# Optimization experiments

Hardware: AMD Instinct MI355X
Metric: run time of the kernel (lower is better)

Reference implementation:

```python
import jax, jax.numpy as jnp
import numpy as np

P = 32    # cardinality (number of parallel paths)
C = 256   # block input/output channels
D = 4     # bottleneck width per path
EPS = 1e-3  # Keras BatchNormalization default epsilon


def setup_inputs() -> dict:
    key = jax.random.key(0)
    ks = jax.random.split(key, 24)
    def nrm(k, shape, s=0.05):
        return jax.random.normal(k, shape, dtype=jnp.float32) * s
    inp = {}
    inp["x"] = jax.random.normal(ks[0], (8, 56, 56, C), dtype=jnp.float32)
    # conv weights/biases, stacked over the path axis P
    inp["W1"] = nrm(ks[1], (P, C, D))          # 1x1 conv C->4
    inp["B1"] = nrm(ks[2], (P, D))
    inp["W2"] = nrm(ks[3], (P, 3, 3, D, D))    # 3x3 conv 4->4 (HWIO)
    inp["B2"] = nrm(ks[4], (P, D))
    inp["W3"] = nrm(ks[5], (P, D, C))          # 1x1 conv 4->256
    inp["B3"] = nrm(ks[6], (P, C))
    # BatchNorm (inference): gamma, beta, moving mean, moving var per stage
    inp["G1"]  = 1.0 + nrm(ks[7], (P, D));  inp["Be1"] = nrm(ks[8], (P, D))
    inp["M1"]  = nrm(ks[9], (P, D));        inp["V1"]  = 1.0 + 0.1 * jax.random.uniform(ks[10], (P, D), dtype=jnp.float32)
    inp["G2"]  = 1.0 + nrm(ks[11], (P, D)); inp["Be2"] = nrm(ks[12], (P, D))
    inp["M2"]  = nrm(ks[13], (P, D));       inp["V2"]  = 1.0 + 0.1 * jax.random.uniform(ks[14], (P, D), dtype=jnp.float32)
    inp["G3"]  = 1.0 + nrm(ks[15], (P, C)); inp["Be3"] = nrm(ks[16], (P, C))
    inp["M3"]  = nrm(ks[17], (P, C));       inp["V3"]  = 1.0 + 0.1 * jax.random.uniform(ks[18], (P, C), dtype=jnp.float32)
    return inp


def _bn(x, g, b, m, v):
    # inference batch-norm: affine over channel axis
    return g * (x - m) * jax.lax.rsqrt(v + EPS) + b


def _path(x, w1, b1, g1, be1, m1, v1, w2, b2, g2, be2, m2, v2, w3, b3, g3, be3, m3, v3):
    h = jnp.einsum('nhwc,cd->nhwd', x, w1) + b1            # 1x1 conv C->D
    h = jax.nn.relu(_bn(h, g1, be1, m1, v1))
    h = jax.lax.conv_general_dilated(
        h, w2, window_strides=(1, 1), padding='SAME',
        dimension_numbers=('NHWC', 'HWIO', 'NHWC')) + b2   # 3x3 conv D->D
    h = jax.nn.relu(_bn(h, g2, be2, m2, v2))
    h = jnp.einsum('nhwd,dc->nhwc', h, w3) + b3            # 1x1 conv D->C
    h = jax.nn.relu(_bn(h, g3, be3, m3, v3))
    return h  # Dropout(0.2) is identity at inference


def reference(x, W1, B1, G1, Be1, M1, V1, W2, B2, G2, Be2, M2, V2, W3, B3, G3, Be3, M3, V3):
    # vmap over the 32 cardinality paths; x is shared (in_axes=None)
    paths = jax.vmap(_path, in_axes=(None,) + (0,) * 18)(
        x, W1, B1, G1, Be1, M1, V1, W2, B2, G2, Be2, M2, V2, W3, B3, G3, Be3, M3, V3)
    return jax.nn.relu(paths.sum(axis=0) + x)
```

## Files before the change

### kernel.cpp

```cpp
#include <hip/hip_runtime.h>

#define BATCH 8
#define HH 56
#define WW 56
#define NPOS (BATCH*HH*WW)
#define C 256
#define P 32
#define D 4
#define J 128
#define EPS 1e-3f
#define H2S 136

typedef __attribute__((ext_vector_type(8))) short bf16x8_t;
typedef __attribute__((ext_vector_type(4))) float f32x4_t;

__device__ __forceinline__ unsigned short f2bf(float f) {
    union { float f; unsigned int i; } v; v.f = f;
    unsigned int r = v.i + 0x7fffu + ((v.i >> 16) & 1u);
    return (unsigned short)(r >> 16);
}
__device__ __forceinline__ uint2 pack4_trunc(float4 v) {
    uint2 r;
    r.x = __builtin_amdgcn_perm(__float_as_uint(v.y), __float_as_uint(v.x), 0x07060302u);
    r.y = __builtin_amdgcn_perm(__float_as_uint(v.w), __float_as_uint(v.z), 0x07060302u);
    return r;
}

__global__ __launch_bounds__(256) void fold_params(
    const float* __restrict__ W1, const float* __restrict__ B1,
    const float* __restrict__ W2, const float* __restrict__ B2,
    const float* __restrict__ W3, const float* __restrict__ B3,
    const float* __restrict__ G1, const float* __restrict__ Be1,
    const float* __restrict__ M1, const float* __restrict__ V1,
    const float* __restrict__ G2, const float* __restrict__ Be2,
    const float* __restrict__ M2, const float* __restrict__ V2,
    const float* __restrict__ G3, const float* __restrict__ Be3,
    const float* __restrict__ M3, const float* __restrict__ V3,
    unsigned short* __restrict__ W1bf, float* __restrict__ b1f,
    float* __restrict__ w2q, float* __restrict__ b2t,
    unsigned short* __restrict__ WB, unsigned short* __restrict__ zb)
{
    int idx = blockIdx.x * 256 + threadIdx.x;

    if (idx < C*J) {
        int j = idx >> 8, c = idx & 255;
        int p = j >> 2, d = j & 3;
        float s = G1[j] * rsqrtf(V1[j] + EPS);
        W1bf[idx] = f2bf(W1[(p*C + c)*D + d] * s);
        return;
    }
    idx -= C*J;
    if (idx < J) {
        float s = G1[idx] * rsqrtf(V1[idx] + EPS);
        b1f[idx] = B1[idx] * s + Be1[idx] - M1[idx] * s;
        return;
    }
    idx -= J;
    if (idx < 9*D*D*P) {
        int do_ = idx & 3, p = (idx >> 2) & 31;
        int r2 = idx >> 7, di = r2 & 3, k9 = r2 >> 2;
        int j = p*4 + do_;
        float s = G2[j] * rsqrtf(V2[j] + EPS);
        w2q[idx] = W2[((p*9 + k9)*4 + di)*4 + do_] * s;
        return;
    }
    idx -= 9*D*D*P;
    if (idx < J) {
        int do_ = idx >> 5, p = idx & 31;
        int j = p*4 + do_;
        float s = G2[j] * rsqrtf(V2[j] + EPS);
        b2t[idx] = B2[j] * s + Be2[j] - M2[j] * s;
        return;
    }
    idx -= J;
    if (idx < P*C*8) {
        int s8 = idx & 7;
        int c = (idx >> 3) & 255;
        int p = idx >> 11;
        float sc = G3[p*C + c] * rsqrtf(V3[p*C + c] + EPS);
        float v = 0.f;
        if (s8 < 4)       v = W3[(p*D + s8)*C + c] * sc;
        else if (s8 == 4) v = B3[p*C + c] * sc + Be3[p*C + c] - M3[p*C + c] * sc;
        WB[idx] = f2bf(v);
        return;
    }
    idx -= P*C*8;
    if (idx < 8) { zb[idx] = 0; return; }
}

__global__ __launch_bounds__(256) void fused_all(
    const float* __restrict__ x, const unsigned short* __restrict__ W1bf,
    const float* __restrict__ b1f, const float* __restrict__ w2q,
    const float* __restrict__ b2t, const unsigned short* __restrict__ WB,
    const unsigned short* __restrict__ zb, float* __restrict__ out)
{
    __shared__ unsigned short xs[64*256];
    __shared__ unsigned short h1L[64*132];
    __shared__ float w2s[4608];
    __shared__ float bs[128];
    __shared__ float b1s[128];
    __shared__ unsigned short h2s[32*H2S];

    const int tid = threadIdx.x;
    int bxx = blockIdx.x;
    const int xb = bxx % 7;  bxx /= 7;
    const int yb = bxx % 14; const int b = bxx / 14;
    const int wid = tid >> 6, l = tid & 63, l15 = l & 15, quad = l >> 4;
    const int j0w = wid * 32;

    union bu { uint4 u; bf16x8_t v; };
    bu aw[2][8];
#pragma unroll
    for (int jf = 0; jf < 2; ++jf) {
        int row = j0w + jf*16 + l15;
#pragma unroll
        for (int kc = 0; kc < 8; ++kc)
            aw[jf][kc].u = *(const uint4*)&W1bf[row*C + kc*32 + quad*8];
    }

    for (int i = tid; i < 4608; i += 256) w2s[i] = w2q[i];
    if (tid < 128) { bs[tid] = b2t[tid]; b1s[tid] = b1f[tid]; }

#pragma unroll
    for (int it = 0; it < 8; ++it) {
        int idx = it*256 + tid;
        int pos = idx >> 5, g = idx & 31;
        uint4 st; st.x = 0u; st.y = 0u; st.z = 0u; st.w = 0u;
        if (pos < 60) {
            int hy = pos / 10, hx = pos - hy*10;
            int gy = yb*4 + hy - 1, gx = xb*8 + hx - 1;
            if (gy >= 0 && gy < HH && gx >= 0 && gx < WW) {
                const float* xp = &x[(size_t)((b*HH + gy)*WW + gx) * C + g*8];
                float4 v0 = *(const float4*)xp;
                float4 v1 = *(const float4*)(xp + 4);
                uint2 p0 = pack4_trunc(v0), p1 = pack4_trunc(v1);
                st.x = p0.x; st.y = p0.y; st.z = p1.x; st.w = p1.y;
            }
        }
        *(uint4*)&xs[pos*256 + ((g ^ (pos & 7)) * 8)] = st;
    }
    __syncthreads();

#pragma unroll
    for (int mt = 0; mt < 4; ++mt) {
        const int row = mt*16 + l15;
        int hy = (row * 205) >> 11;
        int hx = row - hy*10;
        int gy = yb*4 + hy - 1, gx = xb*8 + hx - 1;
        unsigned mask = (row < 60 && gy >= 0 && gy < HH && gx >= 0 && gx < WW)
                        ? 0xFFFFFFFFu : 0u;
        f32x4_t acc0 = (f32x4_t){0.f,0.f,0.f,0.f};
        f32x4_t acc1 = (f32x4_t){0.f,0.f,0.f,0.f};
#pragma unroll
        for (int kc = 0; kc < 8; ++kc) {
            int g = (kc*4 + quad) ^ (row & 7);
            bf16x8_t bb = *(const bf16x8_t*)&xs[row*256 + g*8];
            acc0 = __builtin_amdgcn_mfma_f32_16x16x32_bf16(aw[0][kc].v, bb, acc0, 0, 0, 0);
            acc1 = __builtin_amdgcn_mfma_f32_16x16x32_bf16(aw[1][kc].v, bb, acc1, 0, 0, 0);
        }
#pragma unroll
        for (int jf = 0; jf < 2; ++jf) {
            const f32x4_t a = jf ? acc1 : acc0;
            int jb = j0w + jf*16 + quad*4;
            float4 bias = *(const float4*)&b1s[jb];
            float v0 = fmaxf(a[0] + bias.x, 0.f);
            float v1 = fmaxf(a[1] + bias.y, 0.f);
            float v2 = fmaxf(a[2] + bias.z, 0.f);
            float v3 = fmaxf(a[3] + bias.w, 0.f);
            uint2 o;
            o.x = ((unsigned int)f2bf(v0) | ((unsigned int)f2bf(v1) << 16)) & mask;
            o.y = ((unsigned int)f2bf(v2) | ((unsigned int)f2bf(v3) << 16)) & mask;
            *(uint2*)&h1L[row*132 + jb] = o;
        }
    }
    __syncthreads();

    const int p = tid & 31;
    const int slot = tid >> 5;
    float acc[4][4];
#pragma unroll
    for (int i = 0; i < 4; ++i) {
        acc[i][0] = bs[p]; acc[i][1] = bs[32+p];
        acc[i][2] = bs[64+p]; acc[i][3] = bs[96+p];
    }
#pragma unroll
    for (int ky = 0; ky < 3; ++ky) {
#pragma unroll
        for (int kx = 0; kx < 3; ++kx) {
            const float* wp = &w2s[(ky*3 + kx) * 512 + p*4];
            float4 w0 = *(const float4*)&wp[0];
            float4 w1 = *(const float4*)&wp[128];
            float4 w2v = *(const float4*)&wp[256];
            float4 w3v = *(const float4*)&wp[384];
#pragma unroll
            for (int i = 0; i < 4; ++i) {
                int nl = slot + i*8;
                int hp = ((nl >> 3) + ky)*10 + (nl & 7) + kx;
                uint2 hv = *(const uint2*)&h1L[hp*132 + p*4];
                float f0 = __uint_as_float(hv.x << 16);
                float f1 = __uint_as_float(hv.x & 0xffff0000u);
                float f2 = __uint_as_float(hv.y << 16);
                float f3 = __uint_as_float(hv.y & 0xffff0000u);
                acc[i][0] = fmaf(f0, w0.x, acc[i][0]);  acc[i][1] = fmaf(f0, w0.y, acc[i][1]);
                acc[i][2] = fmaf(f0, w0.z, acc[i][2]);  acc[i][3] = fmaf(f0, w0.w, acc[i][3]);
                acc[i][0] = fmaf(f1, w1.x, acc[i][0]);  acc[i][1] = fmaf(f1, w1.y, acc[i][1]);
                acc[i][2] = fmaf(f1, w1.z, acc[i][2]);  acc[i][3] = fmaf(f1, w1.w, acc[i][3]);
                acc[i][0] = fmaf(f2, w2v.x, acc[i][0]); acc[i][1] = fmaf(f2, w2v.y, acc[i][1]);
                acc[i][2] = fmaf(f2, w2v.z, acc[i][2]); acc[i][3] = fmaf(f2, w2v.w, acc[i][3]);
                acc[i][0] = fmaf(f3, w3v.x, acc[i][0]); acc[i][1] = fmaf(f3, w3v.y, acc[i][1]);
                acc[i][2] = fmaf(f3, w3v.z, acc[i][2]); acc[i][3] = fmaf(f3, w3v.w, acc[i][3]);
            }
        }
    }
#pragma unroll
    for (int i = 0; i < 4; ++i) {
        int nl = slot + i*8;
        uint2 o;
        o.x = (unsigned int)f2bf(fmaxf(acc[i][0], 0.f)) |
              ((unsigned int)f2bf(fmaxf(acc[i][1], 0.f)) << 16);
        o.y = (unsigned int)f2bf(fmaxf(acc[i][2], 0.f)) |
              ((unsigned int)f2bf(fmaxf(acc[i][3], 0.f)) << 16);
        *(uint2*)&h2s[nl*H2S + p*4] = o;
    }
    __syncthreads();

    const int cb = wid * 64;
    const unsigned short* wbp;
    int pstr, cstr;
    if (quad == 0) {
        wbp = &WB[((size_t)(cb + l15)) * 8];
        pstr = C * 8;
        cstr = 16 * 8;
    } else {
        wbp = zb;
        pstr = 0; cstr = 0;
    }

    const f32x4_t zero = (f32x4_t){0.f, 0.f, 0.f, 0.f};
    f32x4_t dacc[2][4];
#pragma unroll
    for (int ps = 0; ps < 2; ++ps)
#pragma unroll
        for (int ct = 0; ct < 4; ++ct) dacc[ps][ct] = zero;
    const unsigned int one = 0x3f80u;

#pragma unroll 2
    for (int pp = 0; pp < 16; ++pp) {
        uint4 h0 = *(const uint4*)&h2s[l15*H2S + pp*8];
        uint4 h1 = *(const uint4*)&h2s[(16 + l15)*H2S + pp*8];
        union au { unsigned int u[4]; bf16x8_t v; };
        au A00, A01, A10, A11;
        A00.u[0] = h0.x; A00.u[1] = h0.y; A00.u[2] = one; A00.u[3] = 0u;
        A01.u[0] = h0.z; A01.u[1] = h0.w; A01.u[2] = one; A01.u[3] = 0u;
        A10.u[0] = h1.x; A10.u[1] = h1.y; A10.u[2] = one; A10.u[3] = 0u;
        A11.u[0] = h1.z; A11.u[1] = h1.w; A11.u[2] = one; A11.u[3] = 0u;
        const unsigned short* pb0 = wbp + pp*2*pstr;
        const unsigned short* pb1 = pb0 + pstr;
#pragma unroll
        for (int ct = 0; ct < 4; ++ct) {
            union bu2 { uint4 u; bf16x8_t v; } B0, B1;
            B0.u = *(const uint4*)(pb0 + ct*cstr);
            B1.u = *(const uint4*)(pb1 + ct*cstr);
            f32x4_t z00 = __builtin_amdgcn_mfma_f32_16x16x32_bf16(A00.v, B0.v, zero, 0, 0, 0);
            f32x4_t z01 = __builtin_amdgcn_mfma_f32_16x16x32_bf16(A01.v, B1.v, zero, 0, 0, 0);
            f32x4_t z10 = __builtin_amdgcn_mfma_f32_16x16x32_bf16(A10.v, B0.v, zero, 0, 0, 0);
            f32x4_t z11 = __builtin_amdgcn_mfma_f32_16x16x32_bf16(A11.v, B1.v, zero, 0, 0, 0);
#pragma unroll
            for (int r = 0; r < 4; ++r) {
                dacc[0][ct][r] += fmaxf(z00[r], 0.f) + fmaxf(z01[r], 0.f);
                dacc[1][ct][r] += fmaxf(z10[r], 0.f) + fmaxf(z11[r], 0.f);
            }
        }
    }

#pragma unroll
    for (int ps = 0; ps < 2; ++ps) {
#pragma unroll
        for (int r = 0; r < 4; ++r) {
            int nl = ps*16 + quad*4 + r;
            int gy = yb*4 + (nl >> 3), gx = xb*8 + (nl & 7);
            size_t n = (size_t)((b*HH + gy)*WW + gx);
            const float* xr = &x[n*C + cb + l15];
            float* orow = &out[n*C + cb + l15];
#pragma unroll
            for (int ct = 0; ct < 4; ++ct) {
                float v = dacc[ps][ct][r] + xr[ct*16];
                orow[ct*16] = fmaxf(v, 0.f);
            }
        }
    }
}

extern "C" void kernel_launch(void* const* d_in, const int* in_sizes, int n_in,
                              void* d_out, int out_size, void* d_ws, size_t ws_size,
                              hipStream_t stream) {
    const float* x  = (const float*)d_in[0];
    const float* W1 = (const float*)d_in[1];
    const float* B1 = (const float*)d_in[2];
    const float* W2 = (const float*)d_in[3];
    const float* B2 = (const float*)d_in[4];
    const float* W3 = (const float*)d_in[5];
    const float* B3 = (const float*)d_in[6];
    const float* G1 = (const float*)d_in[7];
    const float* Be1= (const float*)d_in[8];
    const float* M1 = (const float*)d_in[9];
    const float* V1 = (const float*)d_in[10];
    const float* G2 = (const float*)d_in[11];
    const float* Be2= (const float*)d_in[12];
    const float* M2 = (const float*)d_in[13];
    const float* V2 = (const float*)d_in[14];
    const float* G3 = (const float*)d_in[15];
    const float* Be3= (const float*)d_in[16];
    const float* M3 = (const float*)d_in[17];
    const float* V3 = (const float*)d_in[18];

    char* wsb = (char*)d_ws;
    unsigned short* W1bf = (unsigned short*)(wsb + 0);
    unsigned short* WB   = (unsigned short*)(wsb + 65536);
    float*          w2q  = (float*)(wsb + 196608);
    float*          b1f  = (float*)(wsb + 215040);
    float*          b2t  = (float*)(wsb + 215552);
    unsigned short* zb   = (unsigned short*)(wsb + 216064);

    const int fold_tasks = C*J + J + 9*D*D*P + J + P*C*8 + 8;
    fold_params<<<(fold_tasks + 255)/256, 256, 0, stream>>>(
        W1, B1, W2, B2, W3, B3, G1, Be1, M1, V1, G2, Be2, M2, V2,
        G3, Be3, M3, V3, W1bf, b1f, w2q, b2t, WB, zb);

    fused_all<<<8*14*7, 256, 0, stream>>>(x, W1bf, b1f, w2q, b2t, WB, zb,
                                          (float*)d_out);
}
```

Baseline: 180.5 us.

## Feed stage-1 MFMA directly from global x and drop LDS staging buffers

Removes the shared-memory staging of the x halo tile, w2 weights and biases. The stage-1 MFMA B operands are now loaded straight from global memory and packed to bf16 in registers, and the 3x3 weights and biases are read from global/L2. This cuts LDS use (32KB+18KB) to raise occupancy and removes a sync and an LDS round trip. In exchange the global loads are less coalesced (each lane reads 32B strided chunks) and the weight reads in the 3x3 loop go through cache rather than LDS.

Result: slower. 197.5 us (+9.4%).

```diff
diff --git a/kernel.cpp b/kernel.cpp
--- a/kernel.cpp
+++ b/kernel.cpp
@@ -94,11 +94,7 @@
     const float* __restrict__ b2t, const unsigned short* __restrict__ WB,
     const unsigned short* __restrict__ zb, float* __restrict__ out)
 {
-    __shared__ unsigned short xs[64*256];
     __shared__ unsigned short h1L[64*132];
-    __shared__ float w2s[4608];
-    __shared__ float bs[128];
-    __shared__ float b1s[128];
     __shared__ unsigned short h2s[32*H2S];
 
     const int tid = threadIdx.x;
@@ -118,51 +114,34 @@
             aw[jf][kc].u = *(const uint4*)&W1bf[row*C + kc*32 + quad*8];
     }
 
-    for (int i = tid; i < 4608; i += 256) w2s[i] = w2q[i];
-    if (tid < 128) { bs[tid] = b2t[tid]; b1s[tid] = b1f[tid]; }
-
-#pragma unroll
-    for (int it = 0; it < 8; ++it) {
-        int idx = it*256 + tid;
-        int pos = idx >> 5, g = idx & 31;
-        uint4 st; st.x = 0u; st.y = 0u; st.z = 0u; st.w = 0u;
-        if (pos < 60) {
-            int hy = pos / 10, hx = pos - hy*10;
-            int gy = yb*4 + hy - 1, gx = xb*8 + hx - 1;
-            if (gy >= 0 && gy < HH && gx >= 0 && gx < WW) {
-                const float* xp = &x[(size_t)((b*HH + gy)*WW + gx) * C + g*8];
-                float4 v0 = *(const float4*)xp;
-                float4 v1 = *(const float4*)(xp + 4);
-                uint2 p0 = pack4_trunc(v0), p1 = pack4_trunc(v1);
-                st.x = p0.x; st.y = p0.y; st.z = p1.x; st.w = p1.y;
-            }
-        }
-        *(uint4*)&xs[pos*256 + ((g ^ (pos & 7)) * 8)] = st;
-    }
-    __syncthreads();
-
 #pragma unroll
     for (int mt = 0; mt < 4; ++mt) {
         const int row = mt*16 + l15;
         int hy = (row * 205) >> 11;
         int hx = row - hy*10;
         int gy = yb*4 + hy - 1, gx = xb*8 + hx - 1;
-        unsigned mask = (row < 60 && gy >= 0 && gy < HH && gx >= 0 && gx < WW)
-                        ? 0xFFFFFFFFu : 0u;
+        const bool valid = (row < 60) & (gy >= 0) & (gy < HH) & (gx >= 0) & (gx < WW);
+        const unsigned mask = valid ? 0xFFFFFFFFu : 0u;
+        const size_t n = valid ? (size_t)((b*HH + gy)*WW + gx) : (size_t)0;
+        const float* xp = &x[n*C + quad*8];
+
         f32x4_t acc0 = (f32x4_t){0.f,0.f,0.f,0.f};
         f32x4_t acc1 = (f32x4_t){0.f,0.f,0.f,0.f};
 #pragma unroll
         for (int kc = 0; kc < 8; ++kc) {
-            int g = (kc*4 + quad) ^ (row & 7);
-            bf16x8_t bb = *(const bf16x8_t*)&xs[row*256 + g*8];
-            acc0 = __builtin_amdgcn_mfma_f32_16x16x32_bf16(aw[0][kc].v, bb, acc0, 0, 0, 0);
-            acc1 = __builtin_amdgcn_mfma_f32_16x16x32_bf16(aw[1][kc].v, bb, acc1, 0, 0, 0);
+            float4 v0 = *(const float4*)(xp + kc*32);
+            float4 v1 = *(const float4*)(xp + kc*32 + 4);
+            uint2 p0 = pack4_trunc(v0), p1 = pack4_trunc(v1);
+            union { uint4 u; bf16x8_t v; } bb;
+            bb.u.x = p0.x; bb.u.y = p0.y; bb.u.z = p1.x; bb.u.w = p1.y;
+            acc0 = __builtin_amdgcn_mfma_f32_16x16x32_bf16(aw[0][kc].v, bb.v, acc0, 0, 0, 0);
+            acc1 = __builtin_amdgcn_mfma_f32_16x16x32_bf16(aw[1][kc].v, bb.v, acc1, 0, 0, 0);
         }
 #pragma unroll
         for (int jf = 0; jf < 2; ++jf) {
             const f32x4_t a = jf ? acc1 : acc0;
             int jb = j0w + jf*16 + quad*4;
-            float4 bias = *(const float4*)&b1s[jb];
+            float4 bias = *(const float4*)&b1f[jb];
             float v0 = fmaxf(a[0] + bias.x, 0.f);
             float v1 = fmaxf(a[1] + bias.y, 0.f);
             float v2 = fmaxf(a[2] + bias.z, 0.f);
@@ -178,16 +157,18 @@
     const int p = tid & 31;
     const int slot = tid >> 5;
     float acc[4][4];
-#pragma unroll
-    for (int i = 0; i < 4; ++i) {
-        acc[i][0] = bs[p]; acc[i][1] = bs[32+p];
-        acc[i][2] = bs[64+p]; acc[i][3] = bs[96+p];
+    {
+        float b0 = b2t[p], b1 = b2t[32+p], b2 = b2t[64+p], b3 = b2t[96+p];
+#pragma unroll
+        for (int i = 0; i < 4; ++i) {
+            acc[i][0] = b0; acc[i][1] = b1; acc[i][2] = b2; acc[i][3] = b3;
+        }
     }
 #pragma unroll
     for (int ky = 0; ky < 3; ++ky) {
 #pragma unroll
         for (int kx = 0; kx < 3; ++kx) {
-            const float* wp = &w2s[(ky*3 + kx) * 512 + p*4];
+            const float* wp = &w2q[(ky*3 + kx) * 512 + p*4];
             float4 w0 = *(const float4*)&wp[0];
             float4 w1 = *(const float4*)&wp[128];
             float4 w2v = *(const float4*)&wp[256];
```
